# Kernel tuning notes

Hardware: AMD Instinct MI355X
Metric: run time of the kernel (lower is better)

Reference implementation:

```python
import jax, jax.numpy as jnp
import numpy as np

CLASSES = 128
M_IN = 64
N_OUT = 32
N_SAMPLES = 65536


def setup_inputs() -> dict:
    key = jax.random.key(0)
    k1, k2, k3, k4 = jax.random.split(key, 4)
    x = jax.random.normal(k1, (N_SAMPLES, M_IN), dtype=jnp.float32)
    inds = jax.random.randint(k2, (N_SAMPLES,), 0, CLASSES, dtype=jnp.int64)
    # Conv2d(in=M_IN, out=CLASSES*N_OUT, kernel=1) -> weight (CLASSES*N_OUT, M_IN), bias (CLASSES*N_OUT,)
    bound = 1.0 / np.sqrt(M_IN)
    W = jax.random.uniform(k3, (CLASSES * N_OUT, M_IN), minval=-bound, maxval=bound, dtype=jnp.float32)
    b = jax.random.uniform(k4, (CLASSES * N_OUT,), minval=-bound, maxval=bound, dtype=jnp.float32)
    return {"x": x, "inds": inds, "W": W, "b": b}


def reference(x, inds, W, b):
    # 1x1 conv == GEMM: (N, m) @ (m, classes*n) + bias -> (N, classes*n)
    y = jnp.einsum("nm,cm->nc", x, W) + b  # (N, classes*n_out)
    y = y.reshape(-1, CLASSES, N_OUT)       # (N, classes, n_out)
    # gather the selected class slice per sample
    idx = inds.astype(jnp.int32)[:, None, None]  # (N, 1, 1)
    out = jnp.take_along_axis(y, jnp.broadcast_to(idx, (y.shape[0], 1, N_OUT)), axis=1)
    return out.reshape(-1, N_OUT)
```

## Files before the change

### kernel.cpp

```cpp
#include <hip/hip_runtime.h>

#define CLASSES   128
#define M_IN      64
#define N_OUT     32
#define N_SAMPLES 65536

__global__ __launch_bounds__(256) void condmul_kernel(
    const float* __restrict__ x,
    const int*   __restrict__ inds,
    const float* __restrict__ W,
    const float* __restrict__ b,
    float*       __restrict__ out)
{
    const int waveInBlock = threadIdx.x >> 6;
    const int lane        = threadIdx.x & 63;
    const int n           = (blockIdx.x << 2) + waveInBlock;

    const int m = lane & 15;
    const int q = lane >> 4;

    const int c = __builtin_amdgcn_readfirstlane(inds[n]);

    const float4* __restrict__ Wb =
        reinterpret_cast<const float4*>(W + (size_t)c * (N_OUT * M_IN));
    const float4 xv =
        reinterpret_cast<const float4*>(x + (size_t)n * M_IN)[m];

    float p[8];
#pragma unroll
    for (int i = 0; i < 8; ++i) {
        const float4 w = Wb[i * 64 + lane];
        p[i] = w.x * xv.x + w.y * xv.y + w.z * xv.z + w.w * xv.w;
    }

#pragma unroll
    for (int i = 0; i < 8; ++i) {
#pragma unroll
        for (int off = 8; off >= 1; off >>= 1) {
            p[i] += __shfl_xor(p[i], off, 64);
        }
    }

    __shared__ float lds[4 * N_OUT];
    float* slot = lds + (waveInBlock << 5);
    if (m == 0) {
#pragma unroll
        for (int i = 0; i < 8; ++i) {
            slot[i * 4 + q] = p[i];
        }
    }
    __syncthreads();

    if (lane < N_OUT) {
        const float v = slot[lane] + b[c * N_OUT + lane];
        out[(size_t)n * N_OUT + lane] = v;
    }
}

extern "C" void kernel_launch(void* const* d_in, const int* in_sizes, int n_in,
                              void* d_out, int out_size, void* d_ws, size_t ws_size,
                              hipStream_t stream) {
    const float* x    = (const float*)d_in[0];
    const int*   inds = (const int*)  d_in[1];
    const float* W    = (const float*)d_in[2];
    const float* b    = (const float*)d_in[3];
    float*       out  = (float*)d_out;

    const int block = 256;
    const int grid  = N_SAMPLES / 4;

    condmul_kernel<<<grid, block, 0, stream>>>(x, inds, W, b, out);
}
```

Before: 94.13 us.

## Bucket samples by class and compute per-class with weights staged in LDS

Adds a counting/scatter pass that groups sample indices into per-class buckets, then a compute kernel where each block loads one class's weight matrix into shared memory and processes that class's samples. The goal is to remove repeated global weight fetches per sample. In exchange it adds two extra kernel launches, global atomics, an indirect gather of x and out, per-iteration block barriers, and possible load imbalance across classes.

After: 111.3 us. 18.2% more time.

```diff
diff --git a/kernel.cpp b/kernel.cpp
--- a/kernel.cpp
+++ b/kernel.cpp
@@ -1,59 +1,106 @@
 #include <hip/hip_runtime.h>
 
-#define CLASSES   128
-#define M_IN      64
-#define N_OUT     32
-#define N_SAMPLES 65536
+#define CLASSES    128
+#define M_IN       64
+#define N_OUT      32
+#define N_SAMPLES  65536
+#define BUCKET_CAP N_SAMPLES
 
-__global__ __launch_bounds__(256) void condmul_kernel(
-    const float* __restrict__ x,
-    const int*   __restrict__ inds,
-    const float* __restrict__ W,
-    const float* __restrict__ b,
-    float*       __restrict__ out)
+__global__ __launch_bounds__(128) void zero_cnt_kernel(int* __restrict__ cnt) {
+    cnt[threadIdx.x] = 0;
+}
+
+__global__ __launch_bounds__(256) void scatter_kernel(
+    const int* __restrict__ inds,
+    int*       __restrict__ cnt,
+    int*       __restrict__ bucket)
 {
-    const int waveInBlock = threadIdx.x >> 6;
-    const int lane        = threadIdx.x & 63;
-    const int n           = (blockIdx.x << 2) + waveInBlock;
+    __shared__ int lcnt[CLASSES];
+    __shared__ int lbase[CLASSES];
+    const int tid = threadIdx.x;
+    if (tid < CLASSES) lcnt[tid] = 0;
+    __syncthreads();
 
-    const int m = lane & 15;
-    const int q = lane >> 4;
-
-    const int c = __builtin_amdgcn_readfirstlane(inds[n]);
-
-    const float4* __restrict__ Wb =
-        reinterpret_cast<const float4*>(W + (size_t)c * (N_OUT * M_IN));
-    const float4 xv =
-        reinterpret_cast<const float4*>(x + (size_t)n * M_IN)[m];
-
-    float p[8];
+    int c_k[4], lpos[4], ii[4];
 #pragma unroll
-    for (int i = 0; i < 8; ++i) {
-        const float4 w = Wb[i * 64 + lane];
-        p[i] = w.x * xv.x + w.y * xv.y + w.z * xv.z + w.w * xv.w;
-    }
-
-#pragma unroll
-    for (int i = 0; i < 8; ++i) {
-#pragma unroll
-        for (int off = 8; off >= 1; off >>= 1) {
-            p[i] += __shfl_xor(p[i], off, 64);
-        }
-    }
-
-    __shared__ float lds[4 * N_OUT];
-    float* slot = lds + (waveInBlock << 5);
-    if (m == 0) {
-#pragma unroll
-        for (int i = 0; i < 8; ++i) {
-            slot[i * 4 + q] = p[i];
-        }
+    for (int k = 0; k < 4; ++k) {
+        ii[k]  = blockIdx.x * 1024 + k * 256 + tid;
+        c_k[k] = inds[ii[k]];
+        lpos[k] = atomicAdd(&lcnt[c_k[k]], 1);
     }
     __syncthreads();
 
-    if (lane < N_OUT) {
-        const float v = slot[lane] + b[c * N_OUT + lane];
-        out[(size_t)n * N_OUT + lane] = v;
+    if (tid < CLASSES) lbase[tid] = atomicAdd(&cnt[tid], lcnt[tid]);
+    __syncthreads();
+
+#pragma unroll
+    for (int k = 0; k < 4; ++k) {
+        bucket[c_k[k] * BUCKET_CAP + lbase[c_k[k]] + lpos[k]] = ii[k];
+    }
+}
+
+__global__ __launch_bounds__(256) void compute_kernel(
+    const float* __restrict__ x,
+    const float* __restrict__ W,
+    const float* __restrict__ b,
+    const int*   __restrict__ cnt,
+    const int*   __restrict__ bucket,
+    float*       __restrict__ out)
+{
+    __shared__ float4 Ws4[N_OUT * M_IN / 4];
+    __shared__ float  slots[4 * N_OUT];
+
+    const int c    = blockIdx.x >> 3;
+    const int j    = blockIdx.x & 7;
+    const int tid  = threadIdx.x;
+    const int w    = tid >> 6;
+    const int lane = tid & 63;
+    const int m    = lane & 15;
+    const int q    = lane >> 4;
+
+    const float4* Wb4 = reinterpret_cast<const float4*>(W) + (size_t)c * (N_OUT * M_IN / 4);
+    Ws4[tid]       = Wb4[tid];
+    Ws4[tid + 256] = Wb4[tid + 256];
+
+    const int cntc = cnt[c];
+    __syncthreads();
+
+    const float bv = (lane < N_OUT) ? b[c * N_OUT + lane] : 0.0f;
+    const int   id = j * 4 + w;
+    const int   T  = (cntc + 31) >> 5;
+    float* slot = slots + (w << 5);
+    const float4* x4 = reinterpret_cast<const float4*>(x);
+    const int* bk = bucket + c * BUCKET_CAP;
+
+    for (int t = 0; t < T; ++t) {
+        const int  p     = (t << 5) + id;
+        const bool valid = p < cntc;
+        const int  n     = valid ? bk[p] : 0;
+
+        const float4 xv = x4[(size_t)n * 16 + m];
+
+        float pr[8];
+#pragma unroll
+        for (int i = 0; i < 8; ++i) {
+            const float4 wv = Ws4[i * 64 + lane];
+            pr[i] = wv.x * xv.x + wv.y * xv.y + wv.z * xv.z + wv.w * xv.w;
+        }
+
+#pragma unroll
+        for (int i = 0; i < 8; ++i) {
+#pragma unroll
+            for (int off = 8; off >= 1; off >>= 1)
+                pr[i] += __shfl_xor(pr[i], off, 64);
+        }
+
+        if (m == 0) {
+#pragma unroll
+            for (int i = 0; i < 8; ++i) slot[i * 4 + q] = pr[i];
+        }
+        __syncthreads();
+        if (valid && lane < N_OUT)
+            out[(size_t)n * N_OUT + lane] = slot[lane] + bv;
+        __syncthreads();
     }
 }
 
@@ -66,8 +113,10 @@
     const float* b    = (const float*)d_in[3];
     float*       out  = (float*)d_out;
 
-    const int block = 256;
-    const int grid  = N_SAMPLES / 4;
+    int* cnt    = (int*)d_ws;
+    int* bucket = (int*)d_ws + 1024;
 
-    condmul_kernel<<<grid, block, 0, stream>>>(x, inds, W, b, out);
+    zero_cnt_kernel<<<1, 128, 0, stream>>>(cnt);
+    scatter_kernel<<<N_SAMPLES / 1024, 256, 0, stream>>>(inds, cnt, bucket);
+    compute_kernel<<<CLASSES * 8, 256, 0, stream>>>(x, W, b, cnt, bucket, out);
 }
```
